# Optimization experiments

Measured on AMD Instinct MI355X. Metric: run time of the kernel, lower is better.

The kernel has to match this reference:

```python
import jax, jax.numpy as jnp
import numpy as np
import math

B, H, N, D = 4, 16, 2048, 64
EPS = 1e-8


def setup_inputs() -> dict:
    key = jax.random.key(0)
    kq, kk, kv = jax.random.split(key, 3)
    Q = jax.random.normal(kq, (B, H, N, D), dtype=jnp.float32)
    K = jax.random.normal(kk, (B, H, N, D), dtype=jnp.float32)
    V = jax.random.normal(kv, (B, H, N, D), dtype=jnp.float32)
    # learnable per-head scale, init g0 = log2(N^2 - N)
    g0 = math.log2(N * N - N)
    qk_scale = jnp.full((H,), g0, dtype=jnp.float32)
    # causal mask, broadcast over (B, H)
    M = jnp.tril(jnp.ones((N, N), dtype=bool))
    return {"Q": Q, "K": K, "V": V, "qk_scale": qk_scale, "M": M}


def reference(Q, K, V, qk_scale, M):
    # L2-normalize Q and K along head dim (cosine attention)
    Q_hat = Q / (jnp.sqrt(jnp.sum(Q * Q, axis=-1, keepdims=True)) + EPS)
    K_hat = K / (jnp.sqrt(jnp.sum(K * K, axis=-1, keepdims=True)) + EPS)
    g = qk_scale[None, :, None, None]  # per-head learnable temperature
    scores = jnp.einsum('bhnd,bhmd->bhnm', Q_hat * g, K_hat)
    scores = jnp.where(M, scores, -jnp.inf)
    attn = jax.nn.softmax(scores, axis=-1)  # stable max-subtract softmax
    return jnp.einsum('bhnm,bhmd->bhnd', attn, V)
```

## Files before the change

### kernel.cpp

```cpp
#include <hip/hip_runtime.h>


#define BATCH 4
#define HEADS 16
#define SEQ   2048
#define DIM   64
#define EPS   1e-8f
#define LOG2E 1.44269504088896340736f

typedef short bf16x8 __attribute__((ext_vector_type(8)));
typedef short s16x4  __attribute__((ext_vector_type(4)));
typedef float fx16   __attribute__((ext_vector_type(16)));
typedef unsigned int u32x4 __attribute__((ext_vector_type(4)));

static __device__ __forceinline__ short f2bf(float x) {
    unsigned u = __float_as_uint(x);
    unsigned r = (u + 0x7fffu + ((u >> 16) & 1u)) >> 16;
    return (short)r;
}
static __device__ __forceinline__ unsigned cvt_pk(float lo, float hi) {
    unsigned r;
    asm("v_cvt_pk_bf16_f32 %0, %1, %2" : "=v"(r) : "v"(lo), "v"(hi));
    return r;
}
static __device__ __forceinline__ void gload_lds16(const short* g, short* l) {
    __builtin_amdgcn_global_load_lds(
        (const __attribute__((address_space(1))) void*)g,
        (__attribute__((address_space(3))) void*)l, 16, 0, 0);
}

__global__ __launch_bounds__(256) void norm_k(
    const float* __restrict__ K, short* __restrict__ Kn)
{
    const int tid  = threadIdx.x;
    const int lane = tid & 63;
    long long rid = (long long)blockIdx.x * 16 + (tid >> 6) * 4 + (lane >> 4);
    const int c4 = (lane & 15) * 4;

    const float* src = K + rid * DIM;
    float4 v = *(const float4*)(src + c4);
    float ss = v.x * v.x + v.y * v.y + v.z * v.z + v.w * v.w;
    ss += __shfl_xor(ss, 1);
    ss += __shfl_xor(ss, 2);
    ss += __shfl_xor(ss, 4);
    ss += __shfl_xor(ss, 8);
    float s = 1.0f / (sqrtf(ss) + EPS);

    const int bh = (int)(rid >> 11);
    const int n  = (int)(rid & 2047);
    const int kt = n >> 6;
    const int r  = n & 63;
    short* dst = Kn + ((size_t)bh << 17) + (kt << 12) + (r << 6);

    s16x4 o;
    o[0] = f2bf(v.x * s);
    o[1] = f2bf(v.y * s);
    o[2] = f2bf(v.z * s);
    o[3] = f2bf(v.w * s);
    *(s16x4*)(dst + (c4 ^ ((r & 7) << 3))) = o;
}

#define TLDS 68

__global__ __launch_bounds__(256) void transpose_v(
    const float* __restrict__ V, short* __restrict__ Vt)
{
    const int nt = blockIdx.x;
    const int bh = blockIdx.y;
    const float* Vb = V + ((size_t)bh * SEQ + (size_t)nt * 64) * DIM;
    short* Vo = Vt + ((size_t)bh << 17) + (nt << 12);

    __shared__ short lds[DIM * TLDS];
    const int t  = threadIdx.x;
    const int cg = t & 15;
    const int rr = t >> 4;

#pragma unroll
    for (int i = 0; i < 4; ++i) {
        int n  = rr + i * 16;
        int d0 = cg * 4;
        float4 v = *(const float4*)(Vb + (size_t)n * DIM + d0);
        lds[(d0 + 0) * TLDS + n] = f2bf(v.x);
        lds[(d0 + 1) * TLDS + n] = f2bf(v.y);
        lds[(d0 + 2) * TLDS + n] = f2bf(v.z);
        lds[(d0 + 3) * TLDS + n] = f2bf(v.w);
    }
    __syncthreads();
#pragma unroll
    for (int i = 0; i < 4; ++i) {
        int d  = rr + i * 16;
        int nl = cg * 4;
        s16x4 o;
        o[0] = lds[d * TLDS + nl + 0];
        o[1] = lds[d * TLDS + nl + 1];
        o[2] = lds[d * TLDS + nl + 2];
        o[3] = lds[d * TLDS + nl + 3];
        *(s16x4*)(Vo + (d << 6) + (nl ^ ((d & 7) << 3))) = o;
    }
}

__global__ __launch_bounds__(256) void attn_fwd(
    const float* __restrict__ Q, const float* __restrict__ scale,
    const short* __restrict__ Kn, const short* __restrict__ Vt,
    float* __restrict__ out)
{
    const int lid  = blockIdx.x;
    const int j    = lid & 63;
    const int bh   = (j & 7) * 8 + (j >> 3);
    const int qblk = (SEQ / 128 - 1) - (lid >> 6);
    const int tid  = threadIdx.x;
    const int w    = tid >> 6;
    const int l    = tid & 63;
    const int lq   = l & 31;
    const int hi   = l >> 5;

    const int wlo  = qblk * 128 + w * 32;
    const int whi  = wlo + 31;
    const int qrow = wlo + lq;

    const short* Kb = Kn + ((size_t)bh << 17);
    const short* Vb = Vt + ((size_t)bh << 17);

    __shared__ __align__(16) short ldsK[2][64 * 64];
    __shared__ __align__(16) short ldsV[2][64 * 64];

    {
        const int toff = tid * 8;
        gload_lds16(Kb + toff,        &ldsK[0][toff]);
        gload_lds16(Kb + 2048 + toff, &ldsK[0][2048 + toff]);
        gload_lds16(Vb + toff,        &ldsV[0][toff]);
        gload_lds16(Vb + 2048 + toff, &ldsV[0][2048 + toff]);
    }

    const float* Qrow = Q + ((size_t)bh * SEQ + qrow) * DIM;
    float qv[4][8];
    float ss = 0.f;
#pragma unroll
    for (int c = 0; c < 4; ++c) {
        float4 a = *(const float4*)(Qrow + c * 16 + hi * 8);
        float4 b = *(const float4*)(Qrow + c * 16 + hi * 8 + 4);
        qv[c][0] = a.x; qv[c][1] = a.y; qv[c][2] = a.z; qv[c][3] = a.w;
        qv[c][4] = b.x; qv[c][5] = b.y; qv[c][6] = b.z; qv[c][7] = b.w;
#pragma unroll
        for (int jj = 0; jj < 8; ++jj) ss += qv[c][jj] * qv[c][jj];
    }
    ss += __shfl_xor(ss, 32);
    const float g  = scale[bh & (HEADS - 1)];
    const float sc = g * LOG2E / (sqrtf(ss) + EPS);

    bf16x8 qb[4];
#pragma unroll
    for (int c = 0; c < 4; ++c) {
        u32x4 wds;
#pragma unroll
        for (int m = 0; m < 4; ++m)
            wds[m] = cvt_pk(qv[c][2 * m] * sc, qv[c][2 * m + 1] * sc);
        qb[c] = __builtin_bit_cast(bf16x8, wds);
    }

    fx16 oacc[2];
#pragma unroll
    for (int dt = 0; dt < 2; ++dt)
#pragma unroll
        for (int r = 0; r < 16; ++r) oacc[dt][r] = 0.f;
    float lsum = 0.f;

    const int nkt = 2 * qblk + 2;
    int cur = 0;

    for (int kt = 0; kt < nkt; ++kt) {
        __syncthreads();

        if (kt + 1 < nkt) {
            const int nb = cur ^ 1;
            const int toff = tid * 8;
            const short* gK = Kb + (size_t)(kt + 1) * 4096;
            const short* gV = Vb + (size_t)(kt + 1) * 4096;
            gload_lds16(gK + toff,        &ldsK[nb][toff]);
            gload_lds16(gK + 2048 + toff, &ldsK[nb][2048 + toff]);
            gload_lds16(gV + toff,        &ldsV[nb][toff]);
            gload_lds16(gV + 2048 + toff, &ldsV[nb][2048 + toff]);
        }

        const int k0 = kt * 64;
        if (k0 <= whi) {
            const short* lk = ldsK[cur];
            const short* lv = ldsV[cur];

            fx16 sacc[2];
#pragma unroll
            for (int t = 0; t < 2; ++t)
#pragma unroll
                for (int r = 0; r < 16; ++r) sacc[t][r] = 0.f;

            bf16x8 kf[2][4];
#pragma unroll
            for (int t = 0; t < 2; ++t)
#pragma unroll
                for (int c = 0; c < 4; ++c) {
                    int r = t * 32 + lq;
                    kf[t][c] = *(const bf16x8*)
                        &lk[(r << 6) + ((c * 16 + hi * 8) ^ ((r & 7) << 3))];
                }
            __builtin_amdgcn_s_setprio(1);
#pragma unroll
            for (int c = 0; c < 4; ++c) {
                sacc[0] = __builtin_amdgcn_mfma_f32_32x32x16_bf16(kf[0][c], qb[c], sacc[0], 0, 0, 0);
                sacc[1] = __builtin_amdgcn_mfma_f32_32x32x16_bf16(kf[1][c], qb[c], sacc[1], 0, 0, 0);
            }
            __builtin_amdgcn_s_setprio(0);

            bf16x8 vf[2][4];
#pragma unroll
            for (int dt = 0; dt < 2; ++dt)
#pragma unroll
                for (int ks = 0; ks < 4; ++ks) {
                    int d = dt * 32 + lq;
                    vf[dt][ks] = *(const bf16x8*)
                        &lv[(d << 6) + ((ks * 16 + hi * 8) ^ ((d & 7) << 3))];
                }

            float p[32];
#pragma unroll
            for (int t = 0; t < 2; ++t)
#pragma unroll
                for (int r = 0; r < 16; ++r) p[t * 16 + r] = sacc[t][r];

            if (k0 + 63 > wlo) {
#pragma unroll
                for (int t = 0; t < 2; ++t)
#pragma unroll
                    for (int r = 0; r < 16; ++r) {
                        int key = k0 + 32 * t + (r & 3) + 8 * (r >> 2) + 4 * hi;
                        if (key > qrow) p[t * 16 + r] = -3.0e38f;
                    }
            }

#pragma unroll
            for (int r = 0; r < 32; ++r)
                p[r] = __builtin_amdgcn_exp2f(p[r]);

            float ts[16];
#pragma unroll
            for (int r = 0; r < 16; ++r) ts[r] = p[r] + p[r + 16];
#pragma unroll
            for (int r = 0; r < 8; ++r) ts[r] += ts[r + 8];
#pragma unroll
            for (int r = 0; r < 4; ++r) ts[r] += ts[r + 4];
            float ps = (ts[0] + ts[1]) + (ts[2] + ts[3]);
            ps += __shfl_xor(ps, 32);
            lsum += ps;

            u32x4 paw[4];
#pragma unroll
            for (int ks = 0; ks < 4; ++ks) {
                const int t = ks >> 1;
                const int b0 = (ks & 1) * 8;
#pragma unroll
                for (int m = 0; m < 2; ++m) {
                    unsigned a = cvt_pk(p[t * 16 + b0 + 2 * m], p[t * 16 + b0 + 2 * m + 1]);
                    unsigned b = cvt_pk(p[t * 16 + b0 + 2 * m + 4], p[t * 16 + b0 + 2 * m + 5]);
                    unsigned snd = hi ? a : b;
                    unsigned u = __shfl_xor(snd, 32);
                    paw[ks][m]     = hi ? u : a;
                    paw[ks][m + 2] = hi ? b : u;
                }
            }

            __builtin_amdgcn_s_setprio(1);
#pragma unroll
            for (int dt = 0; dt < 2; ++dt)
#pragma unroll
                for (int ks = 0; ks < 4; ++ks) {
                    bf16x8 pa = __builtin_bit_cast(bf16x8, paw[ks]);
                    oacc[dt] = __builtin_amdgcn_mfma_f32_32x32x16_bf16(vf[dt][ks], pa, oacc[dt], 0, 0, 0);
                }
            __builtin_amdgcn_s_setprio(0);
        }
        cur ^= 1;
    }

    float inv = 1.0f / lsum;
    size_t rb = ((size_t)bh * SEQ + (size_t)qrow) * DIM;
#pragma unroll
    for (int dt = 0; dt < 2; ++dt)
#pragma unroll
        for (int g4 = 0; g4 < 4; ++g4) {
            float4 o4;
            o4.x = oacc[dt][4 * g4 + 0] * inv;
            o4.y = oacc[dt][4 * g4 + 1] * inv;
            o4.z = oacc[dt][4 * g4 + 2] * inv;
            o4.w = oacc[dt][4 * g4 + 3] * inv;
            *(float4*)(out + rb + dt * 32 + 8 * g4 + 4 * hi) = o4;
        }
}

extern "C" void kernel_launch(void* const* d_in, const int* in_sizes, int n_in,
                              void* d_out, int out_size, void* d_ws, size_t ws_size,
                              hipStream_t stream)
{
    const float* Q  = (const float*)d_in[0];
    const float* K  = (const float*)d_in[1];
    const float* V  = (const float*)d_in[2];
    const float* qs = (const float*)d_in[3];
    float* out = (float*)d_out;

    const size_t nElem = (size_t)BATCH * HEADS * SEQ * DIM;
    short* Kn = (short*)d_ws;
    short* Vt = Kn + nElem;

    {
        long long rows = (long long)BATCH * HEADS * SEQ;
        norm_k<<<(int)(rows / 16), 256, 0, stream>>>(K, Kn);
    }
    {
        dim3 grid(SEQ / 64, BATCH * HEADS);
        transpose_v<<<grid, 256, 0, stream>>>(V, Vt);
    }
    {
        attn_fwd<<<(SEQ / 128) * BATCH * HEADS, 256, 0, stream>>>(Q, qs, Kn, Vt, out);
    }
}
```

Baseline: 85.23 us.

## Shrink attention blocks to 64 query rows and use permlane32 swap for P

Query tiles per block shrink from 128 rows (4 waves) to 64 rows (2 waves), doubling the grid so causal work is split more finely. The per-wave causal skip goes away because both waves need every key tile up to the diagonal, and masking now runs only on the last tile. The P repack across half-waves uses v_permlane32_swap in place of shfl_xor plus selects. In exchange, each K/V tile is loaded from global into LDS by twice as many blocks.

```diff
diff --git a/kernel.cpp b/kernel.cpp
--- a/kernel.cpp
+++ b/kernel.cpp
@@ -99,23 +99,21 @@
     }
 }
 
-__global__ __launch_bounds__(256) void attn_fwd(
+__global__ __launch_bounds__(128) void attn_fwd(
     const float* __restrict__ Q, const float* __restrict__ scale,
     const short* __restrict__ Kn, const short* __restrict__ Vt,
     float* __restrict__ out)
 {
-    const int lid  = blockIdx.x;
-    const int j    = lid & 63;
-    const int bh   = (j & 7) * 8 + (j >> 3);
-    const int qblk = (SEQ / 128 - 1) - (lid >> 6);
-    const int tid  = threadIdx.x;
-    const int w    = tid >> 6;
-    const int l    = tid & 63;
-    const int lq   = l & 31;
-    const int hi   = l >> 5;
-
-    const int wlo  = qblk * 128 + w * 32;
-    const int whi  = wlo + 31;
+    const int lid = blockIdx.x;
+    const int bh  = (lid & 7) * 8 + ((lid >> 3) & 7);
+    const int qt  = 31 - (lid >> 6);
+    const int tid = threadIdx.x;
+    const int w   = tid >> 6;
+    const int l   = tid & 63;
+    const int lq  = l & 31;
+    const int hi  = l >> 5;
+
+    const int wlo  = qt * 64 + w * 32;
     const int qrow = wlo + lq;
 
     const short* Kb = Kn + ((size_t)bh << 17);
@@ -124,12 +122,12 @@
     __shared__ __align__(16) short ldsK[2][64 * 64];
     __shared__ __align__(16) short ldsV[2][64 * 64];
 
-    {
-        const int toff = tid * 8;
-        gload_lds16(Kb + toff,        &ldsK[0][toff]);
-        gload_lds16(Kb + 2048 + toff, &ldsK[0][2048 + toff]);
-        gload_lds16(Vb + toff,        &ldsV[0][toff]);
-        gload_lds16(Vb + 2048 + toff, &ldsV[0][2048 + toff]);
+    const int toff = tid * 8;
+
+#pragma unroll
+    for (int s = 0; s < 4; ++s) {
+        gload_lds16(Kb + s * 1024 + toff, &ldsK[0][s * 1024 + toff]);
+        gload_lds16(Vb + s * 1024 + toff, &ldsV[0][s * 1024 + toff]);
     }
 
     const float* Qrow = Q + ((size_t)bh * SEQ + qrow) * DIM;
@@ -165,7 +163,7 @@
         for (int r = 0; r < 16; ++r) oacc[dt][r] = 0.f;
     float lsum = 0.f;
 
-    const int nkt = 2 * qblk + 2;
+    const int nkt = qt + 1;
     int cur = 0;
 
     for (int kt = 0; kt < nkt; ++kt) {
@@ -173,110 +171,108 @@
 
         if (kt + 1 < nkt) {
             const int nb = cur ^ 1;
-            const int toff = tid * 8;
             const short* gK = Kb + (size_t)(kt + 1) * 4096;
             const short* gV = Vb + (size_t)(kt + 1) * 4096;
-            gload_lds16(gK + toff,        &ldsK[nb][toff]);
-            gload_lds16(gK + 2048 + toff, &ldsK[nb][2048 + toff]);
-            gload_lds16(gV + toff,        &ldsV[nb][toff]);
-            gload_lds16(gV + 2048 + toff, &ldsV[nb][2048 + toff]);
+#pragma unroll
+            for (int s = 0; s < 4; ++s) {
+                gload_lds16(gK + s * 1024 + toff, &ldsK[nb][s * 1024 + toff]);
+                gload_lds16(gV + s * 1024 + toff, &ldsV[nb][s * 1024 + toff]);
+            }
         }
 
         const int k0 = kt * 64;
-        if (k0 <= whi) {
-            const short* lk = ldsK[cur];
-            const short* lv = ldsV[cur];
-
-            fx16 sacc[2];
+        const short* lk = ldsK[cur];
+        const short* lv = ldsV[cur];
+
+        fx16 sacc[2];
+#pragma unroll
+        for (int t = 0; t < 2; ++t)
+#pragma unroll
+            for (int r = 0; r < 16; ++r) sacc[t][r] = 0.f;
+
+        bf16x8 kf[2][4];
+#pragma unroll
+        for (int t = 0; t < 2; ++t)
+#pragma unroll
+            for (int c = 0; c < 4; ++c) {
+                int r = t * 32 + lq;
+                kf[t][c] = *(const bf16x8*)
+                    &lk[(r << 6) + ((c * 16 + hi * 8) ^ ((r & 7) << 3))];
+            }
+        __builtin_amdgcn_s_setprio(1);
+#pragma unroll
+        for (int c = 0; c < 4; ++c) {
+            sacc[0] = __builtin_amdgcn_mfma_f32_32x32x16_bf16(kf[0][c], qb[c], sacc[0], 0, 0, 0);
+            sacc[1] = __builtin_amdgcn_mfma_f32_32x32x16_bf16(kf[1][c], qb[c], sacc[1], 0, 0, 0);
+        }
+        __builtin_amdgcn_s_setprio(0);
+
+        bf16x8 vf[2][4];
+#pragma unroll
+        for (int dt = 0; dt < 2; ++dt)
+#pragma unroll
+            for (int ks = 0; ks < 4; ++ks) {
+                int d = dt * 32 + lq;
+                vf[dt][ks] = *(const bf16x8*)
+                    &lv[(d << 6) + ((ks * 16 + hi * 8) ^ ((d & 7) << 3))];
+            }
+
+        float p[32];
+#pragma unroll
+        for (int t = 0; t < 2; ++t)
+#pragma unroll
+            for (int r = 0; r < 16; ++r) p[t * 16 + r] = sacc[t][r];
+
+        if (kt == qt) {
 #pragma unroll
             for (int t = 0; t < 2; ++t)
 #pragma unroll
-                for (int r = 0; r < 16; ++r) sacc[t][r] = 0.f;
-
-            bf16x8 kf[2][4];
-#pragma unroll
-            for (int t = 0; t < 2; ++t)
-#pragma unroll
-                for (int c = 0; c < 4; ++c) {
-                    int r = t * 32 + lq;
-                    kf[t][c] = *(const bf16x8*)
-                        &lk[(r << 6) + ((c * 16 + hi * 8) ^ ((r & 7) << 3))];
+                for (int r = 0; r < 16; ++r) {
+                    int key = k0 + 32 * t + (r & 3) + 8 * (r >> 2) + 4 * hi;
+                    if (key > qrow) p[t * 16 + r] = -3.0e38f;
                 }
-            __builtin_amdgcn_s_setprio(1);
-#pragma unroll
-            for (int c = 0; c < 4; ++c) {
-                sacc[0] = __builtin_amdgcn_mfma_f32_32x32x16_bf16(kf[0][c], qb[c], sacc[0], 0, 0, 0);
-                sacc[1] = __builtin_amdgcn_mfma_f32_32x32x16_bf16(kf[1][c], qb[c], sacc[1], 0, 0, 0);
-            }
-            __builtin_amdgcn_s_setprio(0);
-
-            bf16x8 vf[2][4];
-#pragma unroll
-            for (int dt = 0; dt < 2; ++dt)
-#pragma unroll
-                for (int ks = 0; ks < 4; ++ks) {
-                    int d = dt * 32 + lq;
-                    vf[dt][ks] = *(const bf16x8*)
-                        &lv[(d << 6) + ((ks * 16 + hi * 8) ^ ((d & 7) << 3))];
-                }
-
-            float p[32];
-#pragma unroll
-            for (int t = 0; t < 2; ++t)
-#pragma unroll
-                for (int r = 0; r < 16; ++r) p[t * 16 + r] = sacc[t][r];
-
-            if (k0 + 63 > wlo) {
-#pragma unroll
-                for (int t = 0; t < 2; ++t)
-#pragma unroll
-                    for (int r = 0; r < 16; ++r) {
-                        int key = k0 + 32 * t + (r & 3) + 8 * (r >> 2) + 4 * hi;
-                        if (key > qrow) p[t * 16 + r] = -3.0e38f;
-                    }
-            }
-
-#pragma unroll
-            for (int r = 0; r < 32; ++r)
-                p[r] = __builtin_amdgcn_exp2f(p[r]);
-
-            float ts[16];
-#pragma unroll
-            for (int r = 0; r < 16; ++r) ts[r] = p[r] + p[r + 16];
-#pragma unroll
-            for (int r = 0; r < 8; ++r) ts[r] += ts[r + 8];
-#pragma unroll
-            for (int r = 0; r < 4; ++r) ts[r] += ts[r + 4];
-            float ps = (ts[0] + ts[1]) + (ts[2] + ts[3]);
-            ps += __shfl_xor(ps, 32);
-            lsum += ps;
-
-            u32x4 paw[4];
+        }
+
+#pragma unroll
+        for (int r = 0; r < 32; ++r)
+            p[r] = __builtin_amdgcn_exp2f(p[r]);
+
+        float ts[16];
+#pragma unroll
+        for (int r = 0; r < 16; ++r) ts[r] = p[r] + p[r + 16];
+#pragma unroll
+        for (int r = 0; r < 8; ++r) ts[r] += ts[r + 8];
+#pragma unroll
+        for (int r = 0; r < 4; ++r) ts[r] += ts[r + 4];
+        float ps = (ts[0] + ts[1]) + (ts[2] + ts[3]);
+        ps += __shfl_xor(ps, 32);
+        lsum += ps;
+
+        u32x4 paw[4];
+#pragma unroll
+        for (int ks = 0; ks < 4; ++ks) {
+            const int t = ks >> 1;
+            const int b0 = (ks & 1) * 8;
+#pragma unroll
+            for (int m = 0; m < 2; ++m) {
+                unsigned a = cvt_pk(p[t * 16 + b0 + 2 * m], p[t * 16 + b0 + 2 * m + 1]);
+                unsigned b = cvt_pk(p[t * 16 + b0 + 2 * m + 4], p[t * 16 + b0 + 2 * m + 5]);
+                asm("v_permlane32_swap_b32 %0, %1" : "+v"(a), "+v"(b));
+                paw[ks][m]     = a;
+                paw[ks][m + 2] = b;
+            }
+        }
+
+        __builtin_amdgcn_s_setprio(1);
+#pragma unroll
+        for (int dt = 0; dt < 2; ++dt)
 #pragma unroll
             for (int ks = 0; ks < 4; ++ks) {
-                const int t = ks >> 1;
-                const int b0 = (ks & 1) * 8;
-#pragma unroll
-                for (int m = 0; m < 2; ++m) {
-                    unsigned a = cvt_pk(p[t * 16 + b0 + 2 * m], p[t * 16 + b0 + 2 * m + 1]);
-                    unsigned b = cvt_pk(p[t * 16 + b0 + 2 * m + 4], p[t * 16 + b0 + 2 * m + 5]);
-                    unsigned snd = hi ? a : b;
-                    unsigned u = __shfl_xor(snd, 32);
-                    paw[ks][m]     = hi ? u : a;
-                    paw[ks][m + 2] = hi ? b : u;
-                }
-            }
-
-            __builtin_amdgcn_s_setprio(1);
-#pragma unroll
-            for (int dt = 0; dt < 2; ++dt)
-#pragma unroll
-                for (int ks = 0; ks < 4; ++ks) {
-                    bf16x8 pa = __builtin_bit_cast(bf16x8, paw[ks]);
-                    oacc[dt] = __builtin_amdgcn_mfma_f32_32x32x16_bf16(vf[dt][ks], pa, oacc[dt], 0, 0, 0);
-                }
-            __builtin_amdgcn_s_setprio(0);
-        }
+                bf16x8 pa = __builtin_bit_cast(bf16x8, paw[ks]);
+                oacc[dt] = __builtin_amdgcn_mfma_f32_32x32x16_bf16(vf[dt][ks], pa, oacc[dt], 0, 0, 0);
+            }
+        __builtin_amdgcn_s_setprio(0);
+
         cur ^= 1;
     }
 
@@ -318,6 +314,6 @@
         transpose_v<<<grid, 256, 0, stream>>>(V, Vt);
     }
     {
-        attn_fwd<<<(SEQ / 128) * BATCH * HEADS, 256, 0, stream>>>(Q, qs, Kn, Vt, out);
-    }
-}
+        attn_fwd<<<(SEQ / 64) * BATCH * HEADS, 128, 0, stream>>>(Q, qs, Kn, Vt, out);
+    }
+}
```

Measured after the change: 86.43 us. Within noise of the previous version (+1.4%).
